# Kernel tuning notes

Hardware: AMD Instinct MI355X
Metric: run time of the kernel (lower is better)

The kernel has to match this reference:

```python
import jax, jax.numpy as jnp
import numpy as np

NUM_E = 20000   # entities
NUM_R = 200     # relations (rel table has 2*NUM_R rows)
H = 200         # h_dim
TD = 48         # t_dim (UnionTimeEncode: two halves of 24)
HD = TD // 2
L_HIST = 32     # padded per-(batch,k) history list length
HIS_K = 3
N_HIST = 3      # len(his_list_g)
N_LAYERS = 2    # RGCN layers (config.num_layers)
E = 200000      # edges per historical graph
BATCH = 512


def setup_inputs() -> dict:
    key = jax.random.key(0)
    ks = jax.random.split(key, 32)
    nrm = lambda k, shape, s=0.05: (jax.random.normal(k, shape, jnp.float32) * s)
    inp = {}
    # graph / index inputs (int)
    inp['src'] = jax.random.randint(ks[0], (N_HIST, E), 0, NUM_E, jnp.int32)
    inp['dst'] = jax.random.randint(ks[1], (N_HIST, E), 0, NUM_E, jnp.int32)
    inp['etype'] = jax.random.randint(ks[2], (N_HIST, E), 0, 2 * NUM_R, jnp.int32)
    inp['data'] = jax.random.randint(ks[3], (BATCH, 4), 0, NUM_R, jnp.int32)  # s,r,o,t
    inp['his_idx'] = jax.random.randint(ks[4], (BATCH, HIS_K, L_HIST), 0, NUM_E, jnp.int32)
    inp['his_len'] = jax.random.randint(ks[5], (BATCH, HIS_K), 0, L_HIST + 1, jnp.int32)
    # parameters (float)
    inp['ent'] = nrm(ks[6], (NUM_E, H), 0.5)          # EntEmb.ent (normal init)
    inp['loop_weight'] = nrm(ks[7], (H, H))           # EntEmb self-loop weight
    inp['rel'] = nrm(ks[8], (2 * NUM_R, H), 0.5)
    # UnionTimeEncode params (AbsTimeEncode v=0 + CosTimeEncode)
    basis = (1.0 / 10 ** np.linspace(0.0, 9.0, HD)).astype(np.float32)
    inp['abs_freq'] = jnp.asarray(basis)
    inp['abs_phase'] = jnp.zeros((HD,), jnp.float32)
    inp['cos_freq'] = jnp.asarray(basis)
    inp['cos_phase'] = jnp.zeros((HD,), jnp.float32)
    # RGCN (RE-GCN style Union-RGCN layer: msg=(h_src+rel_e)@Wn, mean agg, self-loop)
    inp['Wn'] = nrm(ks[9], (N_LAYERS, H, H))
    inp['Ws'] = nrm(ks[10], (N_LAYERS, H, H))
    # GRUCell (PyTorch layout)
    inp['W_ih'] = nrm(ks[11], (3 * H, H + TD))
    inp['W_hh'] = nrm(ks[12], (3 * H, H))
    inp['b_ih'] = jnp.zeros((3 * H,), jnp.float32)
    inp['b_hh'] = jnp.zeros((3 * H,), jnp.float32)
    # attention fusion
    inp['Wb_w'] = nrm(ks[13], (H, 3 * H + TD))
    inp['Wb_b'] = jnp.zeros((H,), jnp.float32)
    inp['Wc_w'] = nrm(ks[14], (1, H))
    inp['Wc_b'] = jnp.zeros((1,), jnp.float32)
    # decoder (MLP query @ entity table)
    inp['Wd_w'] = nrm(ks[15], (H, 3 * H))
    inp['Wd_b'] = jnp.zeros((H,), jnp.float32)
    return inp


def _l2n(x, eps=1e-12):
    # F.normalize: x / max(||x||, eps)
    n = jnp.linalg.norm(x, axis=-1, keepdims=True)
    return x / jnp.maximum(n, eps)


def reference(src, dst, etype, data, his_idx, his_len,
              ent, loop_weight, rel, abs_freq, abs_phase, cos_freq, cos_phase,
              Wn, Ws, W_ih, W_hh, b_ih, b_hh, Wb_w, Wb_b, Wc_w, Wc_b, Wd_w, Wd_b):
    def tenc(t):  # t: [N,1] float -> [N,TD]
        a = jnp.tanh((t + 1.0) * abs_freq + abs_phase)   # AbsTimeEncode(act=tanh)
        c = jnp.cos(t * cos_freq + cos_phase)            # CosTimeEncode
        return jnp.concatenate([a, c], axis=1)

    s_i, r_i = data[:, 0], data[:, 1]
    ent_e = ent @ loop_weight                  # EntEmb self-loop (dropout=identity, eval)
    rel_n = _l2n(rel)
    prev = _l2n(ent_e)                         # g_list[0]
    tim_cnt = N_HIST
    ones_e = jnp.ones((E,), jnp.float32)
    for i in range(N_HIST):                    # python loop over fixed #graphs
        si, di, ei = src[i], dst[i], etype[i]
        deg = jax.ops.segment_sum(ones_e, di, num_segments=NUM_E)         # in-degree
        inv = 1.0 / jnp.maximum(deg, 1.0)
        # g.update_all(copy_src, mean): zero in-degree nodes -> 0
        agg = jax.ops.segment_sum(prev[si], di, num_segments=NUM_E) * inv[:, None]
        h = _l2n(jnp.where(deg[:, None] > 0, agg, 0.0))
        tim_cnt -= 1
        tim = jnp.where(deg > 0, float(tim_cnt), 100.0)[:, None]
        te = tenc(tim)                                                     # [NUM_E,TD]
        for l in range(N_LAYERS):              # RGCN
            msg = (h[si] + rel_n[ei]) @ Wn[l]                              # [E,H]
            nagg = jax.ops.segment_sum(msg, di, num_segments=NUM_E) * inv[:, None]
            h = jax.nn.relu(nagg + h @ Ws[l])
        h = _l2n(h)
        # GRUCell(cat([h, te]), prev)
        gi = jnp.concatenate([h, te], axis=1) @ W_ih.T + b_ih
        gh = prev @ W_hh.T + b_hh
        ir, iz, iN = jnp.split(gi, 3, axis=1)
        hr, hz, hN = jnp.split(gh, 3, axis=1)
        rg = jax.nn.sigmoid(ir + hr)
        zg = jax.nn.sigmoid(iz + hz)
        ng = jnp.tanh(iN + rg * hN)
        prev = _l2n((1.0 - zg) * ng + zg * prev)
    out = prev

    q_s, q_r = out[s_i], rel_n[r_i]
    tim_cnt = min(N_HIST, HIS_K)
    s_embs, atts = [], []
    pos = jnp.arange(L_HIST)[None, :]
    for k in range(min(N_HIST, HIS_K)):
        tim_cnt -= 1
        ln = his_len[:, k]
        mask = (pos < ln[:, None]).astype(jnp.float32)                     # [B,L]
        # sparse one-hot mm + divide by length
        tmp = jnp.einsum('blh,bl->bh', out[his_idx[:, k, :]], mask)
        tmp = _l2n(tmp / jnp.maximum(ln, 1).astype(jnp.float32)[:, None])
        tim = jnp.where(ln > 0, float(tim_cnt), 100.0)[:, None]
        te = tenc(tim)                                                     # [B,TD]
        s_embs.append(tmp)
        a = jax.nn.relu(jnp.concatenate([q_s, q_r, tmp, te], 1) @ Wb_w.T + Wb_b)
        atts.append(a @ Wc_w.T + Wc_b)                                     # [B,1]
    att = jax.nn.softmax(jnp.stack(atts, axis=1), axis=1)                  # [B,K,1]
    out2 = jnp.sum(jnp.stack(s_embs, axis=1) * att, axis=1)                # bmm fusion
    # decoder: MLP query scored against all entity states
    q = jax.nn.relu(jnp.concatenate([q_s, q_r, out2], 1) @ Wd_w.T + Wd_b)
    return q @ out.T                                                       # [B,NUM_E]
```

## Files before the change

kernel.cpp:

```cpp
#include <hip/hip_runtime.h>
#include <hip/hip_bf16.h>

#define NUM_E   20000
#define H_DIM   200
#define TD_DIM  48
#define HD_DIM  24
#define L_HIST  32
#define N_HIST  3
#define E_EDGES 200000
#define BATCH   512


__device__ inline float wave_sum64(float x) {
    #pragma unroll
    for (int m = 1; m < 64; m <<= 1) x += __shfl_xor(x, m);
    return x;
}

__device__ inline ushort f2bf(float f) {
    unsigned u = __float_as_uint(f);
    u += 0x7fffu + ((u >> 16) & 1u);
    return (ushort)(u >> 16);
}
__device__ inline float bf2f(ushort u) {
    return __uint_as_float(((unsigned)u) << 16);
}
__device__ inline float4 bf4_to_f4(ushort4 v) {
    return (float4){bf2f(v.x), bf2f(v.y), bf2f(v.z), bf2f(v.w)};
}

__global__ void fill_i32(int* __restrict__ p, long n, int v) {
    long i = (long)blockIdx.x * blockDim.x + threadIdx.x;
    if (i < n) p[i] = v;
}

__global__ void bias_sum(float* __restrict__ bsum, const float* __restrict__ b_ih,
                         const float* __restrict__ b_hh) {
    int j = blockIdx.x * 256 + threadIdx.x;
    if (j < 600) bsum[j] = b_ih[j] + b_hh[j];
}

__global__ void cvt_bf16_k(ushort* __restrict__ o, const float* __restrict__ in, long n) {
    long i = (long)blockIdx.x * 256 + threadIdx.x;
    if (i < n) o[i] = f2bf(in[i]);
}

__global__ void make_lo(ushort* __restrict__ lo, const float* __restrict__ x,
                        const ushort* __restrict__ hi, long n) {
    long i = (long)blockIdx.x * 256 + threadIdx.x;
    if (i < n) lo[i] = f2bf(x[i] - bf2f(hi[i]));
}

__global__ void tcvt_bf16_k(ushort* __restrict__ o, const float* __restrict__ in, int R, int C) {
    int i = blockIdx.x * 256 + threadIdx.x;
    if (i >= R * C) return;
    int r = i / C, c = i - r * C;
    o[(size_t)c * R + r] = f2bf(in[i]);
}

struct Segs {
    const float* A[4];
    const float* B[4];
    int lda[4], ldb[4], Ks[4];
    int nseg, Ktot;
};

__device__ inline void seg_find(const Segs& sg, int gk, int& s, int& loc) {
    s = 0; loc = gk;
    #pragma unroll
    for (int t = 0; t < 3; t++) {
        if (s + 1 < sg.nseg && loc >= sg.Ks[s]) { loc -= sg.Ks[s]; s++; }
    }
}

__global__ __launch_bounds__(256) void sgemm_splitk(
    float* __restrict__ P, const Segs sg, int M, int N, int nbx, int nby,
    int KS, int tpc)
{
    __shared__ float As[32][68];
    __shared__ float Bs[32][68];

    int tot = nbx * nby;
    int tot_all = tot * KS;
    int chunk = (tot_all + 7) >> 3;
    int v = (int)(blockIdx.x & 7) * chunk + (int)(blockIdx.x >> 3);
    if (v >= tot_all) return;
    int kc = v / tot;
    int tile = v - kc * tot;
    int by = tile / nbx, bx = tile - by * nbx;
    const int bn = bx * 64;
    const int bm = by * 64;
    const int tid = threadIdx.x;
    const int m0 = (tid >> 4) * 4;
    const int n0 = (tid & 15) * 4;

    float acc[4][4];
    #pragma unroll
    for (int i = 0; i < 4; i++)
        #pragma unroll
        for (int j = 0; j < 4; j++) acc[i][j] = 0.f;

    const int Ktot = sg.Ktot;
    const int ntile = (Ktot + 31) / 32;
    const int kt0 = kc * tpc;
    const int kt1 = min(ntile, kt0 + tpc);

    const int a_m  = tid & 31;
    const int a_k4 = (tid >> 5) * 4;
    const int b1_n = tid & 63;
    const int b1_k = (tid >> 6) * 4;

    float4 ra[2], rb[2];
    auto loadA = [&](int k0) {
        int gk = k0 + a_k4;
        bool kin = gk < Ktot;
        int s = 0, loc = 0;
        if (kin) seg_find(sg, gk, s, loc);
        const float* Ab = sg.A[s];
        const int lda = sg.lda[s];
        #pragma unroll
        for (int r = 0; r < 2; r++) {
            int row = bm + a_m + 32 * r;
            float4 vv = {0.f, 0.f, 0.f, 0.f};
            if (kin && row < M) vv = *(const float4*)(Ab + (size_t)row * lda + loc);
            ra[r] = vv;
        }
    };
    auto loadB = [&](int k0) {
        #pragma unroll
        for (int r = 0; r < 2; r++) {
            int k4 = b1_k + 16 * r;
            int gk = k0 + k4;
            bool kin = gk < Ktot;
            int s = 0, loc = 0;
            if (kin) seg_find(sg, gk, s, loc);
            const float* Bb = sg.B[s];
            const int ldb = sg.ldb[s];
            int gn = bn + b1_n;
            float4 vv = {0.f, 0.f, 0.f, 0.f};
            if (kin && gn < N) vv = *(const float4*)(Bb + (size_t)gn * ldb + loc);
            rb[r] = vv;
        }
    };

    if (kt0 < kt1) {
        loadA(kt0 * 32); loadB(kt0 * 32);
        for (int t = kt0; t < kt1; t++) {
            #pragma unroll
            for (int r = 0; r < 2; r++) {
                int m = a_m + 32 * r;
                As[a_k4 + 0][m] = ra[r].x;
                As[a_k4 + 1][m] = ra[r].y;
                As[a_k4 + 2][m] = ra[r].z;
                As[a_k4 + 3][m] = ra[r].w;
            }
            #pragma unroll
            for (int r = 0; r < 2; r++) {
                int k4 = b1_k + 16 * r;
                Bs[k4 + 0][b1_n] = rb[r].x;
                Bs[k4 + 1][b1_n] = rb[r].y;
                Bs[k4 + 2][b1_n] = rb[r].z;
                Bs[k4 + 3][b1_n] = rb[r].w;
            }
            __syncthreads();
            if (t + 1 < kt1) { loadA((t + 1) * 32); loadB((t + 1) * 32); }
            #pragma unroll 8
            for (int kk = 0; kk < 32; kk++) {
                float4 b = *(float4*)&Bs[kk][n0];
                float4 av = *(float4*)&As[kk][m0];
                float a[4] = {av.x, av.y, av.z, av.w};
                #pragma unroll
                for (int i = 0; i < 4; i++) {
                    acc[i][0] += a[i] * b.x;
                    acc[i][1] += a[i] * b.y;
                    acc[i][2] += a[i] * b.z;
                    acc[i][3] += a[i] * b.w;
                }
            }
            __syncthreads();
        }
    }

    int col = bn + n0;
    if (col < N) {
        #pragma unroll
        for (int i = 0; i < 4; i++) {
            int row = bm + m0 + i;
            if (row < M) {
                float4 o = {acc[i][0], acc[i][1], acc[i][2], acc[i][3]};
                *(float4*)(P + ((size_t)kc * M + row) * N + col) = o;
            }
        }
    }
}

__global__ void reduce_relu(float* __restrict__ out, const float* __restrict__ P,
                            const float* __restrict__ bias, int MN, int N, int KS)
{
    int i = blockIdx.x * 256 + threadIdx.x;
    if (i >= MN) return;
    float s = bias[i % N];
    for (int k = 0; k < KS; k++) s += P[(size_t)k * MN + i];
    out[i] = fmaxf(s, 0.f);
}

__global__ void reduce_relu_split(ushort* __restrict__ qhi, ushort* __restrict__ qlo,
                                  const float* __restrict__ P, const float* __restrict__ bias,
                                  int MN, int N, int KS)
{
    int i = blockIdx.x * 256 + threadIdx.x;
    if (i >= MN) return;
    float s = bias[i % N];
    for (int k = 0; k < KS; k++) s += P[(size_t)k * MN + i];
    s = fmaxf(s, 0.f);
    ushort h = f2bf(s);
    qhi[i] = h;
    qlo[i] = f2bf(s - bf2f(h));
}

typedef __attribute__((ext_vector_type(8))) short bfrag;
typedef __attribute__((ext_vector_type(4))) float ffrag;

struct BfSegs {
    const ushort* A[3];
    const ushort* B[3];
    int lda[3], ldb[3], Ks[3];
    int nseg, Ktot;
};

__device__ inline void bseg_find(const BfSegs& sg, int gk, int& s, int& loc) {
    s = 0; loc = gk;
    #pragma unroll
    for (int t = 0; t < 2; t++) {
        if (s + 1 < sg.nseg && loc >= sg.Ks[s]) { loc -= sg.Ks[s]; s++; }
    }
}

struct GemmDesc {
    BfSegs sg;
    float* C;
    ushort* Cb;
    const float* bias;
    int M, N, ldc;
    int act, flags, order;
    int nbx, nby, blk0, nblk;
};

struct MultiArgs {
    GemmDesc d[3];
    int nd;
    int tot;
};

template<int DI>
__device__ __forceinline__ void gemm_body(const MultiArgs& ma, int v,
                                          ushort* __restrict__ Als,
                                          ushort* __restrict__ Bls)
{
    const GemmDesc& D = ma.d[DI];
    const BfSegs& sg = D.sg;
    const int tile = v - D.blk0;
    int by, bx;
    if (D.order == 0) { by = tile / D.nbx; bx = tile - by * D.nbx; }
    else              { bx = tile / D.nby; by = tile - bx * D.nby; }
    const int bm = by * 64, bn = bx * 64;
    const int M = D.M, N = D.N;

    const int tid  = threadIdx.x;
    const int lane = tid & 63;
    const int w    = tid >> 6;
    const int wm   = (w & 1) * 2;
    const int wn   = (w >> 1) * 2;

    ffrag acc[2][2];
    #pragma unroll
    for (int i = 0; i < 2; i++)
        #pragma unroll
        for (int j = 0; j < 2; j++) acc[i][j] = (ffrag){0.f, 0.f, 0.f, 0.f};

    const int Ktot = sg.Ktot;
    const int nkt = (Ktot + 63) >> 6;

    int a_m[2], a_kq[2], a_wc[2];
    #pragma unroll
    for (int i = 0; i < 2; i++) {
        int c = i * 256 + tid;
        a_m[i] = c & 63; a_kq[i] = c >> 6;
        a_wc[i] = ((a_m[i] >> 4) * 2 + (a_kq[i] >> 2)) * 64 + (a_kq[i] & 3) * 16 + (a_m[i] & 15);
    }
    int b_n[2], b_kq[2], b_wc[2];
    #pragma unroll
    for (int i = 0; i < 2; i++) {
        int c = i * 256 + tid;
        b_n[i] = c & 63; b_kq[i] = c >> 6;
        b_wc[i] = ((b_n[i] >> 4) * 2 + (b_kq[i] >> 2)) * 64 + (b_kq[i] & 3) * 16 + (b_n[i] & 15);
    }

    uint4 ra[2], rb[2];
    auto loadA = [&](int k0) {
        #pragma unroll
        for (int i = 0; i < 2; i++) {
            int gk = k0 + a_kq[i] * 8;
            int row = bm + a_m[i];
            uint4 vv = {0u, 0u, 0u, 0u};
            if (gk < Ktot && row < M) {
                int s, loc; bseg_find(sg, gk, s, loc);
                vv = *(const uint4*)(sg.A[s] + (size_t)row * sg.lda[s] + loc);
            }
            ra[i] = vv;
        }
    };
    auto loadB = [&](int k0) {
        #pragma unroll
        for (int i = 0; i < 2; i++) {
            int gk = k0 + b_kq[i] * 8;
            int gn = bn + b_n[i];
            uint4 vv = {0u, 0u, 0u, 0u};
            if (gk < Ktot && gn < N) {
                int s, loc; bseg_find(sg, gk, s, loc);
                vv = *(const uint4*)(sg.B[s] + (size_t)gn * sg.ldb[s] + loc);
            }
            rb[i] = vv;
        }
    };

    loadA(0); loadB(0);

    for (int t = 0; t < nkt; t++) {
        #pragma unroll
        for (int i = 0; i < 2; i++) *(uint4*)(&Als[a_wc[i] * 8]) = ra[i];
        #pragma unroll
        for (int i = 0; i < 2; i++) *(uint4*)(&Bls[b_wc[i] * 8]) = rb[i];
        __syncthreads();

        if (t + 1 < nkt) { loadA((t + 1) << 6); loadB((t + 1) << 6); }

        #pragma unroll
        for (int kt = 0; kt < 2; kt++) {
            bfrag af[2], bf[2];
            #pragma unroll
            for (int i = 0; i < 2; i++)
                af[i] = *(const bfrag*)(&Als[(((wm + i) * 2 + kt) * 64 + lane) * 8]);
            #pragma unroll
            for (int j = 0; j < 2; j++)
                bf[j] = *(const bfrag*)(&Bls[(((wn + j) * 2 + kt) * 64 + lane) * 8]);
            #pragma unroll
            for (int i = 0; i < 2; i++)
                #pragma unroll
                for (int j = 0; j < 2; j++)
                    acc[i][j] = __builtin_amdgcn_mfma_f32_16x16x32_bf16(af[i], bf[j], acc[i][j], 0, 0, 0);
        }
        __syncthreads();
    }

    const int rbase = (lane >> 4) * 4;
    const int cl = lane & 15;
    #pragma unroll
    for (int j = 0; j < 2; j++) {
        int col = bn + (wn + j) * 16 + cl;
        if (col >= N) continue;
        float bv = D.bias ? D.bias[col] : 0.f;
        #pragma unroll
        for (int i = 0; i < 2; i++) {
            int mrow = bm + (wm + i) * 16 + rbase;
            #pragma unroll
            for (int r = 0; r < 4; r++) {
                int row = mrow + r;
                if (row < M) {
                    float o = acc[i][j][r] + bv;
                    if (D.act == 1) o = fmaxf(o, 0.f);
                    else if (D.act == 2) o = 1.f / (1.f + expf(-o));
                    if (D.flags & 1) D.C[(size_t)row * D.ldc + col] = o;
                    if (D.flags & 2) D.Cb[(size_t)row * D.ldc + col] = f2bf(o);
                }
            }
        }
    }
}

__global__ __launch_bounds__(256) void mfma_multi(MultiArgs ma)
{
    __shared__ __align__(16) ushort Als[4096];
    __shared__ __align__(16) ushort Bls[4096];

    int tot = ma.tot;
    int chunk = (tot + 7) >> 3;
    int v = (int)(blockIdx.x & 7) * chunk + (int)(blockIdx.x >> 3);
    if (v >= tot) return;

    int di = 0;
    if (ma.nd > 1 && v >= ma.d[1].blk0) di = 1;
    if (ma.nd > 2 && v >= ma.d[2].blk0) di = 2;

    if (di == 0)      gemm_body<0>(ma, v, Als, Bls);
    else if (di == 1) gemm_body<1>(ma, v, Als, Bls);
    else              gemm_body<2>(ma, v, Als, Bls);
}


__global__ void count_dst(const int* __restrict__ di, int* __restrict__ cnt, int E) {
    int e = blockIdx.x * 256 + threadIdx.x;
    if (e < E) atomicAdd(&cnt[di[e]], 1);
}

__global__ __launch_bounds__(1024) void scan_rows(
    const int* __restrict__ cnt, int* __restrict__ row_start, int* __restrict__ cursor,
    float* __restrict__ degf, float* __restrict__ invd)
{
    __shared__ int part[1024];
    const int CH = (NUM_E + 1023) / 1024;
    int t = threadIdx.x;
    int base = t * CH;
    int local[32];
    int s = 0;
    for (int j = 0; j < CH; j++) {
        int idx = base + j;
        int c = (idx < NUM_E) ? cnt[idx] : 0;
        local[j] = s; s += c;
    }
    part[t] = s;
    __syncthreads();
    for (int off = 1; off < 1024; off <<= 1) {
        int vv = (t >= off) ? part[t - off] : 0;
        __syncthreads();
        part[t] += vv;
        __syncthreads();
    }
    int pre = (t == 0) ? 0 : part[t - 1];
    for (int j = 0; j < CH; j++) {
        int idx = base + j;
        if (idx < NUM_E) {
            int rs = pre + local[j];
            row_start[idx] = rs;
            cursor[idx] = rs;
            int c = cnt[idx];
            degf[idx] = (float)c;
            invd[idx] = 1.f / fmaxf((float)c, 1.f);
        }
    }
    if (t == 1023) row_start[NUM_E] = part[1023];
}

__global__ void build_perm(const int* __restrict__ si, const int* __restrict__ di,
                           const int* __restrict__ ei, int* __restrict__ cursor,
                           int* __restrict__ ssrc, int* __restrict__ setype, int E)
{
    int e = blockIdx.x * 256 + threadIdx.x;
    if (e >= E) return;
    int pos = atomicAdd(&cursor[di[e]], 1);
    ssrc[pos]   = si[e];
    setype[pos] = ei[e];
}


__global__ __launch_bounds__(256) void seg_gather_norm_bf(
    ushort* __restrict__ bh, const ushort* __restrict__ bprev,
    const int* __restrict__ ssrc, const int* __restrict__ row_start,
    const float* __restrict__ invd)
{
    int v = blockIdx.x * 4 + (threadIdx.x >> 6);
    int lane = threadIdx.x & 63;
    if (v >= NUM_E) return;
    int s0 = row_start[v], s1 = row_start[v + 1];
    bool act = lane < 50;
    float4 acc = {0.f, 0.f, 0.f, 0.f};
    int j = s0;
    for (; j + 1 < s1; j += 2) {
        int sa = ssrc[j], sb = ssrc[j + 1];
        if (act) {
            float4 xa = bf4_to_f4(*(const ushort4*)(bprev + (long)sa * H_DIM + lane * 4));
            float4 xb = bf4_to_f4(*(const ushort4*)(bprev + (long)sb * H_DIM + lane * 4));
            acc.x += xa.x + xb.x; acc.y += xa.y + xb.y;
            acc.z += xa.z + xb.z; acc.w += xa.w + xb.w;
        }
    }
    if (j < s1) {
        int sa = ssrc[j];
        if (act) {
            float4 xa = bf4_to_f4(*(const ushort4*)(bprev + (long)sa * H_DIM + lane * 4));
            acc.x += xa.x; acc.y += xa.y; acc.z += xa.z; acc.w += xa.w;
        }
    }
    float iv = invd[v];
    acc.x *= iv; acc.y *= iv; acc.z *= iv; acc.w *= iv;
    float ss = act ? (acc.x*acc.x + acc.y*acc.y + acc.z*acc.z + acc.w*acc.w) : 0.f;
    ss = wave_sum64(ss);
    float r = 1.f / fmaxf(sqrtf(ss), 1e-12f);
    if (act) {
        ushort4 ob = {f2bf(acc.x * r), f2bf(acc.y * r), f2bf(acc.z * r), f2bf(acc.w * r)};
        *(ushort4*)(bh + (long)v * H_DIM + lane * 4) = ob;
    }
}

__global__ __launch_bounds__(256) void seg_gather_layer_bf(
    ushort* __restrict__ btmp, const ushort* __restrict__ bh, const ushort* __restrict__ brel,
    const int* __restrict__ ssrc, const int* __restrict__ setype,
    const int* __restrict__ row_start, const float* __restrict__ invd)
{
    int v = blockIdx.x * 4 + (threadIdx.x >> 6);
    int lane = threadIdx.x & 63;
    if (v >= NUM_E) return;
    int s0 = row_start[v], s1 = row_start[v + 1];
    bool act = lane < 50;
    float4 acc = {0.f, 0.f, 0.f, 0.f};
    int j = s0;
    for (; j + 1 < s1; j += 2) {
        int sa = ssrc[j], ta = setype[j];
        int sb = ssrc[j + 1], tb = setype[j + 1];
        if (act) {
            float4 xa = bf4_to_f4(*(const ushort4*)(bh   + (long)sa * H_DIM + lane * 4));
            float4 ya = bf4_to_f4(*(const ushort4*)(brel + (long)ta * H_DIM + lane * 4));
            float4 xb = bf4_to_f4(*(const ushort4*)(bh   + (long)sb * H_DIM + lane * 4));
            float4 yb = bf4_to_f4(*(const ushort4*)(brel + (long)tb * H_DIM + lane * 4));
            acc.x += (xa.x + ya.x) + (xb.x + yb.x);
            acc.y += (xa.y + ya.y) + (xb.y + yb.y);
            acc.z += (xa.z + ya.z) + (xb.z + yb.z);
            acc.w += (xa.w + ya.w) + (xb.w + yb.w);
        }
    }
    if (j < s1) {
        int s = ssrc[j];
        int t = setype[j];
        if (act) {
            float4 x = bf4_to_f4(*(const ushort4*)(bh   + (long)s * H_DIM + lane * 4));
            float4 y = bf4_to_f4(*(const ushort4*)(brel + (long)t * H_DIM + lane * 4));
            acc.x += x.x + y.x; acc.y += x.y + y.y;
            acc.z += x.z + y.z; acc.w += x.w + y.w;
        }
    }
    float iv = invd[v];
    if (act) {
        ushort4 ob = {f2bf(acc.x * iv), f2bf(acc.y * iv), f2bf(acc.z * iv), f2bf(acc.w * iv)};
        *(ushort4*)(btmp + (long)v * H_DIM + lane * 4) = ob;
    }
}


__global__ __launch_bounds__(256) void l2norm_rows4(
    float* __restrict__ out, ushort* __restrict__ bout,
    const float* __restrict__ in, int nrows)
{
    int v = blockIdx.x * 4 + (threadIdx.x >> 6);
    int lane = threadIdx.x & 63;
    if (v >= nrows) return;
    bool act = lane < 50;
    float4 x = {0.f, 0.f, 0.f, 0.f};
    if (act) x = *(const float4*)(in + (long)v * H_DIM + lane * 4);
    float ss = x.x*x.x + x.y*x.y + x.z*x.z + x.w*x.w;
    ss = wave_sum64(ss);
    float r = 1.f / fmaxf(sqrtf(ss), 1e-12f);
    if (act) {
        long base = (long)v * H_DIM + lane * 4;
        float4 o = {x.x * r, x.y * r, x.z * r, x.w * r};
        *(float4*)(out + base) = o;
        if (bout) {
            ushort4 ob = {f2bf(o.x), f2bf(o.y), f2bf(o.z), f2bf(o.w)};
            *(ushort4*)(bout + base) = ob;
        }
    }
}

__global__ __launch_bounds__(256) void l2norm_bf4(ushort* __restrict__ b, int nrows)
{
    int v = blockIdx.x * 4 + (threadIdx.x >> 6);
    int lane = threadIdx.x & 63;
    if (v >= nrows) return;
    bool act = lane < 50;
    float4 x = {0.f, 0.f, 0.f, 0.f};
    long base = (long)v * H_DIM + lane * 4;
    if (act) x = bf4_to_f4(*(const ushort4*)(b + base));
    float ss = x.x*x.x + x.y*x.y + x.z*x.z + x.w*x.w;
    ss = wave_sum64(ss);
    float r = 1.f / fmaxf(sqrtf(ss), 1e-12f);
    if (act) {
        ushort4 ob = {f2bf(x.x * r), f2bf(x.y * r), f2bf(x.z * r), f2bf(x.w * r)};
        *(ushort4*)(b + base) = ob;
    }
}

__global__ void tenc_table(ushort* __restrict__ tbl, const float* __restrict__ af,
                           const float* __restrict__ ap, const float* __restrict__ cf,
                           const float* __restrict__ cp, float tcnt)
{
    int j = threadIdx.x;
    if (j >= 128) return;
    int half = j >> 6;
    int jj = j & 63;
    if (jj >= TD_DIM) return;
    float t = half ? 100.0f : tcnt;
    float val;
    if (jj < HD_DIM) val = tanhf((t + 1.f) * af[jj] + ap[jj]);
    else             val = cosf(t * cf[jj - HD_DIM] + cp[jj - HD_DIM]);
    tbl[half * 64 + jj] = f2bf(val);
}

__global__ void tenc_fill(ushort* __restrict__ bte, const float* __restrict__ deg,
                          const ushort* __restrict__ tbl, int M)
{
    int idx = blockIdx.x * 256 + threadIdx.x;
    if (idx >= M * 6) return;
    int v = idx / 6, c = idx - v * 6;
    int base = (deg[v] > 0.f) ? 0 : 64;
    *(uint4*)(bte + (long)v * TD_DIM + c * 8) = *(const uint4*)(tbl + base + c * 8);
}

__global__ __launch_bounds__(256) void gru_fused(
    float* __restrict__ prev, ushort* __restrict__ bprev, const float* __restrict__ rz,
    const float* __restrict__ iN, const float* __restrict__ hN)
{
    int v = blockIdx.x * 4 + (threadIdx.x >> 6);
    int lane = threadIdx.x & 63;
    if (v >= NUM_E) return;
    bool act = lane < 50;
    long b200 = (long)v * H_DIM + lane * 4;
    long b400 = (long)v * 400 + lane * 4;
    float4 o = {0.f, 0.f, 0.f, 0.f};
    if (act) {
        float4 r4 = *(const float4*)(rz + b400);
        float4 z4 = *(const float4*)(rz + b400 + 200);
        float4 n4 = *(const float4*)(iN + b200);
        float4 g4 = *(const float4*)(hN + b200);
        float4 p4 = *(const float4*)(prev + b200);
        float ngx = tanhf(n4.x + r4.x * g4.x);
        float ngy = tanhf(n4.y + r4.y * g4.y);
        float ngz = tanhf(n4.z + r4.z * g4.z);
        float ngw = tanhf(n4.w + r4.w * g4.w);
        o.x = (1.f - z4.x) * ngx + z4.x * p4.x;
        o.y = (1.f - z4.y) * ngy + z4.y * p4.y;
        o.z = (1.f - z4.z) * ngz + z4.z * p4.z;
        o.w = (1.f - z4.w) * ngw + z4.w * p4.w;
    }
    float ss = o.x*o.x + o.y*o.y + o.z*o.z + o.w*o.w;
    ss = wave_sum64(ss);
    float r = 1.f / fmaxf(sqrtf(ss), 1e-12f);
    if (act) {
        float4 wv = {o.x * r, o.y * r, o.z * r, o.w * r};
        *(float4*)(prev + b200) = wv;
        ushort4 ob = {f2bf(wv.x), f2bf(wv.y), f2bf(wv.z), f2bf(wv.w)};
        *(ushort4*)(bprev + b200) = ob;
    }
}


__global__ void gather_qs_qr3(float* __restrict__ qs3, float* __restrict__ qr3,
                              const float* __restrict__ out, const float* __restrict__ reln,
                              const int* __restrict__ data)
{
    long i = (long)blockIdx.x * 256 + threadIdx.x;
    if (i >= (long)BATCH * H_DIM) return;
    int b = (int)(i / H_DIM), j = (int)(i % H_DIM);
    float vs = out[(long)data[b * 4 + 0] * H_DIM + j];
    float vr = reln[(long)data[b * 4 + 1] * H_DIM + j];
    const long S = (long)BATCH * H_DIM;
    qs3[i] = vs; qs3[i + S] = vs; qs3[i + 2*S] = vs;
    qr3[i] = vr; qr3[i + S] = vr; qr3[i + 2*S] = vr;
}

__global__ __launch_bounds__(64) void semb_kernel(
    float* __restrict__ semb, const float* __restrict__ out,
    const int* __restrict__ his_idx, const int* __restrict__ his_len)
{
    int b = blockIdx.x, k = blockIdx.y;
    int lane = threadIdx.x;
    int ln = his_len[b * 3 + k];
    if (ln > L_HIST) ln = L_HIST;
    float vals[4] = {0.f, 0.f, 0.f, 0.f};
    for (int l = 0; l < ln; l++) {
        int idx = his_idx[((long)b * 3 + k) * L_HIST + l];
        #pragma unroll
        for (int t = 0; t < 4; t++) {
            int j = lane + t * 64;
            if (j < H_DIM) vals[t] += out[(long)idx * H_DIM + j];
        }
    }
    float scale = 1.f / fmaxf((float)ln, 1.f);
    float ss = 0.f;
    #pragma unroll
    for (int t = 0; t < 4; t++) { vals[t] *= scale; ss += vals[t] * vals[t]; }
    ss = wave_sum64(ss);
    float r = 1.f / fmaxf(sqrtf(ss), 1e-12f);
    #pragma unroll
    for (int t = 0; t < 4; t++) {
        int j = lane + t * 64;
        if (j < H_DIM) semb[((long)k * BATCH + b) * H_DIM + j] = vals[t] * r;
    }
}

__global__ void tenc_batch(float* __restrict__ teb, const int* __restrict__ his_len,
                           const float* __restrict__ af, const float* __restrict__ ap,
                           const float* __restrict__ cf, const float* __restrict__ cp)
{
    int idx = blockIdx.x * 256 + threadIdx.x;
    if (idx >= 3 * BATCH * TD_DIM) return;
    int k = idx / (BATCH * TD_DIM);
    int rem = idx - k * (BATCH * TD_DIM);
    int b = rem / TD_DIM, j = rem % TD_DIM;
    int ln = his_len[b * 3 + k];
    float t = (ln > 0) ? (float)(2 - k) : 100.0f;
    float val;
    if (j < HD_DIM) val = tanhf((t + 1.f) * af[j] + ap[j]);
    else            val = cosf(t * cf[j - HD_DIM] + cp[j - HD_DIM]);
    teb[idx] = val;
}

__global__ __launch_bounds__(256) void att_logits_rows(
    float* __restrict__ atts, const float* __restrict__ a,
    const float* __restrict__ Wc_w, const float* __restrict__ Wc_b)
{
    int row = blockIdx.x * 4 + (threadIdx.x >> 6);
    int lane = threadIdx.x & 63;
    if (row >= 3 * BATCH) return;
    int k = row >> 9;
    int b = row & 511;
    float s = 0.f;
    for (int j = lane; j < H_DIM; j += 64) s += a[(long)row * H_DIM + j] * Wc_w[j];
    s = wave_sum64(s);
    if (lane == 0) atts[b * 3 + k] = s + Wc_b[0];
}

__global__ void softmax_out2(float* __restrict__ out2, const float* __restrict__ atts,
                             const float* __restrict__ semb)
{
    long i = (long)blockIdx.x * 256 + threadIdx.x;
    if (i >= (long)BATCH * H_DIM) return;
    int b = (int)(i / H_DIM), j = (int)(i % H_DIM);
    float l0 = atts[b * 3 + 0], l1 = atts[b * 3 + 1], l2 = atts[b * 3 + 2];
    float m = fmaxf(l0, fmaxf(l1, l2));
    float e0 = expf(l0 - m), e1 = expf(l1 - m), e2 = expf(l2 - m);
    float s = e0 + e1 + e2;
    float v = (e0 * semb[((long)0 * BATCH + b) * H_DIM + j] +
               e1 * semb[((long)1 * BATCH + b) * H_DIM + j] +
               e2 * semb[((long)2 * BATCH + b) * H_DIM + j]) / s;
    out2[i] = v;
}


extern "C" void kernel_launch(void* const* d_in, const int* in_sizes, int n_in,
                              void* d_out, int out_size, void* d_ws, size_t ws_size,
                              hipStream_t stream)
{
    (void)in_sizes; (void)n_in; (void)out_size; (void)ws_size;

    const int*   src     = (const int*)d_in[0];
    const int*   dst     = (const int*)d_in[1];
    const int*   etype   = (const int*)d_in[2];
    const int*   data    = (const int*)d_in[3];
    const int*   his_idx = (const int*)d_in[4];
    const int*   his_len = (const int*)d_in[5];
    const float* ent     = (const float*)d_in[6];
    const float* loop_w  = (const float*)d_in[7];
    const float* rel     = (const float*)d_in[8];
    const float* af      = (const float*)d_in[9];
    const float* ap      = (const float*)d_in[10];
    const float* cf      = (const float*)d_in[11];
    const float* cp      = (const float*)d_in[12];
    const float* Wn      = (const float*)d_in[13];
    const float* Ws      = (const float*)d_in[14];
    const float* W_ih    = (const float*)d_in[15];
    const float* W_hh    = (const float*)d_in[16];
    const float* b_ih    = (const float*)d_in[17];
    const float* b_hh    = (const float*)d_in[18];
    const float* Wb_w    = (const float*)d_in[19];
    const float* Wb_b    = (const float*)d_in[20];
    const float* Wc_w    = (const float*)d_in[21];
    const float* Wc_b    = (const float*)d_in[22];
    const float* Wd_w    = (const float*)d_in[23];
    const float* Wd_b    = (const float*)d_in[24];
    float* out_p = (float*)d_out;

    float* wp = (float*)d_ws;
    size_t off = 0;
    auto alloc = [&](size_t n) {
        size_t n4 = (n + 3) & ~(size_t)3;
        float* p = wp + off; off += n4; return p;
    };
    const long nE200 = (long)NUM_E * H_DIM;
    float* prev   = alloc(nE200);
    float* h1     = alloc(nE200);
    float* tmp    = alloc(nE200);
    float* rz     = out_p;
    ushort* bh0   = (ushort*)alloc(nE200 / 2);
    ushort* bh1   = (ushort*)alloc(nE200 / 2);
    ushort* btmp  = (ushort*)alloc(nE200 / 2);
    ushort* bprev = (ushort*)alloc(nE200 / 2);
    ushort* plo   = (ushort*)alloc(nE200 / 2);
    ushort* bte   = (ushort*)alloc((size_t)NUM_E * TD_DIM / 2);
    ushort* brel  = (ushort*)alloc(400 * H_DIM / 2);
    ushort* bW_ih = (ushort*)alloc(600 * 248 / 2);
    ushort* bW_hh = (ushort*)alloc(600 * 200 / 2);
    ushort* bWn_t = (ushort*)alloc(2 * 200 * 200 / 2);
    ushort* bWs_t = (ushort*)alloc(2 * 200 * 200 / 2);
    ushort* bLp_t = (ushort*)alloc(200 * 200 / 2);
    ushort* qhi   = (ushort*)alloc(BATCH * H_DIM / 2);
    ushort* qlo   = (ushort*)alloc(BATCH * H_DIM / 2);
    ushort* ttbl  = (ushort*)alloc(64);
    float* degf   = alloc(NUM_E);
    float* invd   = alloc(NUM_E);
    float* reln   = alloc(400 * H_DIM);
    float* bsum   = alloc(1024);
    float* qs3    = alloc(3 * BATCH * H_DIM);
    float* qr3    = alloc(3 * BATCH * H_DIM);
    float* semb   = alloc(3 * BATCH * H_DIM);
    float* teb    = alloc(3 * BATCH * TD_DIM);
    float* abuf   = alloc(3 * BATCH * H_DIM);
    float* atts   = alloc(2048);
    float* out2   = alloc(BATCH * H_DIM);
    int* cnt       = (int*)alloc(NUM_E);
    int* row_start = (int*)alloc(NUM_E + 4);
    int* cursor    = (int*)alloc(NUM_E);
    int* ssrc      = (int*)alloc(E_EDGES);
    int* setype    = (int*)alloc(E_EDGES);

    auto nblk = [](long n) { return (unsigned)((n + 255) / 256); };

    auto bseg1 = [](const ushort* A, int la, const ushort* B, int lb, int K) {
        BfSegs s{}; s.A[0]=A; s.lda[0]=la; s.B[0]=B; s.ldb[0]=lb; s.Ks[0]=K;
        s.nseg=1; s.Ktot=K; return s;
    };
    auto bseg2 = [](const ushort* A0, int la0, const ushort* B0, int lb0, int K0,
                    const ushort* A1, int la1, const ushort* B1, int lb1, int K1) {
        BfSegs s{}; s.A[0]=A0; s.lda[0]=la0; s.B[0]=B0; s.ldb[0]=lb0; s.Ks[0]=K0;
        s.A[1]=A1; s.lda[1]=la1; s.B[1]=B1; s.ldb[1]=lb1; s.Ks[1]=K1;
        s.nseg=2; s.Ktot=K0+K1; return s;
    };
    auto bseg3 = [](const ushort* A0, int la0, const ushort* B0, int lb0, int K0,
                    const ushort* A1, int la1, const ushort* B1, int lb1, int K1,
                    const ushort* A2, int la2, const ushort* B2, int lb2, int K2) {
        BfSegs s{}; s.A[0]=A0; s.lda[0]=la0; s.B[0]=B0; s.ldb[0]=lb0; s.Ks[0]=K0;
        s.A[1]=A1; s.lda[1]=la1; s.B[1]=B1; s.ldb[1]=lb1; s.Ks[1]=K1;
        s.A[2]=A2; s.lda[2]=la2; s.B[2]=B2; s.ldb[2]=lb2; s.Ks[2]=K2;
        s.nseg=3; s.Ktot=K0+K1+K2; return s;
    };

    auto desc = [](const BfSegs& sg, float* C, ushort* Cb, const float* bias,
                   int M, int N, int ldc, int act, int flags, int order) {
        GemmDesc D{}; D.sg=sg; D.C=C; D.Cb=Cb; D.bias=bias;
        D.M=M; D.N=N; D.ldc=ldc; D.act=act; D.flags=flags; D.order=order;
        D.nbx=(N+63)>>6; D.nby=(M+63)>>6; D.nblk=D.nbx*D.nby; D.blk0=0;
        return D;
    };
    auto launch_multi = [&](GemmDesc* ds, int nd) {
        MultiArgs ma{};
        int tot = 0;
        for (int i = 0; i < nd; i++) { ds[i].blk0 = tot; tot += ds[i].nblk; ma.d[i] = ds[i]; }
        ma.nd = nd; ma.tot = tot;
        unsigned grid = (unsigned)(((tot + 7) >> 3) << 3);
        mfma_multi<<<grid, 256, 0, stream>>>(ma);
    };

    auto seg3 = [](const float* A0, int la0, const float* B0, int lb0, int K0,
                   const float* A1, int la1, const float* B1, int lb1, int K1,
                   const float* A2, int la2, const float* B2, int lb2, int K2) {
        Segs s{}; s.A[0]=A0; s.lda[0]=la0; s.B[0]=B0; s.ldb[0]=lb0; s.Ks[0]=K0;
        s.A[1]=A1; s.lda[1]=la1; s.B[1]=B1; s.ldb[1]=lb1; s.Ks[1]=K1;
        s.A[2]=A2; s.lda[2]=la2; s.B[2]=B2; s.ldb[2]=lb2; s.Ks[2]=K2;
        s.nseg=3; s.Ktot=K0+K1+K2; return s;
    };
    auto seg4 = [](const float* A0, int la0, const float* B0, int lb0, int K0,
                   const float* A1, int la1, const float* B1, int lb1, int K1,
                   const float* A2, int la2, const float* B2, int lb2, int K2,
                   const float* A3, int la3, const float* B3, int lb3, int K3) {
        Segs s{}; s.A[0]=A0; s.lda[0]=la0; s.B[0]=B0; s.ldb[0]=lb0; s.Ks[0]=K0;
        s.A[1]=A1; s.lda[1]=la1; s.B[1]=B1; s.ldb[1]=lb1; s.Ks[1]=K1;
        s.A[2]=A2; s.lda[2]=la2; s.B[2]=B2; s.ldb[2]=lb2; s.Ks[2]=K2;
        s.A[3]=A3; s.lda[3]=la3; s.B[3]=B3; s.ldb[3]=lb3; s.Ks[3]=K3;
        s.nseg=4; s.Ktot=K0+K1+K2+K3; return s;
    };
    auto splitk = [&](float* P, const Segs& sg, int M, int N, int KS) {
        int nbx = (N + 63) >> 6;
        int nby = (M + 63) >> 6;
        int ntile = (sg.Ktot + 31) / 32;
        int tpc = (ntile + KS - 1) / KS;
        int tot_all = nbx * nby * KS;
        unsigned grid = (unsigned)(((tot_all + 7) >> 3) << 3);
        sgemm_splitk<<<grid, 256, 0, stream>>>(P, sg, M, N, nbx, nby, KS, tpc);
    };

    const unsigned r4 = (NUM_E + 3) / 4;

    l2norm_rows4<<<100, 256, 0, stream>>>(reln, brel, rel, 400);
    bias_sum<<<3, 256, 0, stream>>>(bsum, b_ih, b_hh);
    cvt_bf16_k<<<nblk(600L*248), 256, 0, stream>>>(bW_ih, W_ih, 600L*248);
    cvt_bf16_k<<<nblk(600L*200), 256, 0, stream>>>(bW_hh, W_hh, 600L*200);
    tcvt_bf16_k<<<nblk(40000), 256, 0, stream>>>(bLp_t, loop_w, 200, 200);
    tcvt_bf16_k<<<nblk(40000), 256, 0, stream>>>(bWn_t,          Wn,          200, 200);
    tcvt_bf16_k<<<nblk(40000), 256, 0, stream>>>(bWn_t + 40000,  Wn + 40000,  200, 200);
    tcvt_bf16_k<<<nblk(40000), 256, 0, stream>>>(bWs_t,          Ws,          200, 200);
    tcvt_bf16_k<<<nblk(40000), 256, 0, stream>>>(bWs_t + 40000,  Ws + 40000,  200, 200);

    cvt_bf16_k<<<nblk(nE200), 256, 0, stream>>>(btmp, ent, nE200);
    {
        GemmDesc d0 = desc(bseg1(btmp, H_DIM, bLp_t, H_DIM, H_DIM),
                           tmp, nullptr, nullptr, NUM_E, H_DIM, H_DIM, 0, 1, 0);
        launch_multi(&d0, 1);
    }
    l2norm_rows4<<<r4, 256, 0, stream>>>(prev, bprev, tmp, NUM_E);

    for (int i = 0; i < N_HIST; i++) {
        const int* si = src   + (long)i * E_EDGES;
        const int* di = dst   + (long)i * E_EDGES;
        const int* ei = etype + (long)i * E_EDGES;
        float tcnt = (float)(N_HIST - 1 - i);

        fill_i32<<<nblk(NUM_E), 256, 0, stream>>>(cnt, NUM_E, 0);
        count_dst<<<nblk(E_EDGES), 256, 0, stream>>>(di, cnt, E_EDGES);
        scan_rows<<<1, 1024, 0, stream>>>(cnt, row_start, cursor, degf, invd);
        build_perm<<<nblk(E_EDGES), 256, 0, stream>>>(si, di, ei, cursor, ssrc, setype, E_EDGES);

        seg_gather_norm_bf<<<r4, 256, 0, stream>>>(bh0, bprev, ssrc, row_start, invd);
        tenc_table<<<1, 128, 0, stream>>>(ttbl, af, ap, cf, cp, tcnt);
        tenc_fill<<<nblk((long)NUM_E * 6), 256, 0, stream>>>(bte, degf, ttbl, NUM_E);

        seg_gather_layer_bf<<<r4, 256, 0, stream>>>(btmp, bh0, brel, ssrc, setype, row_start, invd);
        {
            GemmDesc d0 = desc(bseg2(btmp, H_DIM, bWn_t,         H_DIM, H_DIM,
                                     bh0,  H_DIM, bWs_t,         H_DIM, H_DIM),
                               nullptr, bh1, nullptr, NUM_E, H_DIM, H_DIM, 1, 2, 0);
            launch_multi(&d0, 1);
        }
        seg_gather_layer_bf<<<r4, 256, 0, stream>>>(btmp, bh1, brel, ssrc, setype, row_start, invd);
        {
            GemmDesc d0 = desc(bseg2(btmp, H_DIM, bWn_t + 40000, H_DIM, H_DIM,
                                     bh1,  H_DIM, bWs_t + 40000, H_DIM, H_DIM),
                               nullptr, bh0, nullptr, NUM_E, H_DIM, H_DIM, 1, 2, 0);
            launch_multi(&d0, 1);
        }
        l2norm_bf4<<<r4, 256, 0, stream>>>(bh0, NUM_E);

        {
            GemmDesc d3[3];
            d3[0] = desc(bseg3(bh0,   H_DIM,  bW_ih,       248, H_DIM,
                               bte,   TD_DIM, bW_ih + 200, 248, TD_DIM,
                               bprev, H_DIM,  bW_hh,       200, H_DIM),
                         rz, nullptr, bsum, NUM_E, 400, 400, 2, 1, 0);
            d3[1] = desc(bseg2(bh0, H_DIM,  bW_ih + 400*248,       248, H_DIM,
                               bte, TD_DIM, bW_ih + 400*248 + 200, 248, TD_DIM),
                         h1, nullptr, b_ih + 400, NUM_E, H_DIM, H_DIM, 0, 1, 0);
            d3[2] = desc(bseg1(bprev, H_DIM, bW_hh + 400*200, 200, H_DIM),
                         tmp, nullptr, b_hh + 400, NUM_E, H_DIM, H_DIM, 0, 1, 0);
            launch_multi(d3, 3);
        }

        gru_fused<<<r4, 256, 0, stream>>>(prev, bprev, rz, h1, tmp);
    }

    gather_qs_qr3<<<nblk((long)BATCH * H_DIM), 256, 0, stream>>>(qs3, qr3, prev, reln, data);
    semb_kernel<<<dim3(BATCH, 3), 64, 0, stream>>>(semb, prev, his_idx, his_len);
    tenc_batch<<<nblk(3L * BATCH * TD_DIM), 256, 0, stream>>>(teb, his_len, af, ap, cf, cp);

    {
        const int KS = 8;
        const int MN = 3 * BATCH * H_DIM;
        splitk(h1, seg4(qs3, H_DIM,  Wb_w,       648, H_DIM,
                        qr3, H_DIM,  Wb_w + 200, 648, H_DIM,
                        semb, H_DIM, Wb_w + 400, 648, H_DIM,
                        teb, TD_DIM, Wb_w + 600, 648, TD_DIM),
               3 * BATCH, H_DIM, KS);
        reduce_relu<<<nblk(MN), 256, 0, stream>>>(abuf, h1, Wb_b, MN, H_DIM, KS);
    }
    att_logits_rows<<<(3 * BATCH + 3) / 4, 256, 0, stream>>>(atts, abuf, Wc_w, Wc_b);
    softmax_out2<<<nblk((long)BATCH * H_DIM), 256, 0, stream>>>(out2, atts, semb);

    {
        const int KS = 8;
        const int MN = BATCH * H_DIM;
        splitk(tmp, seg3(qs3, H_DIM,  Wd_w,       600, H_DIM,
                         qr3, H_DIM,  Wd_w + 200, 600, H_DIM,
                         out2, H_DIM, Wd_w + 400, 600, H_DIM),
               BATCH, H_DIM, KS);
        reduce_relu_split<<<nblk(MN), 256, 0, stream>>>(qhi, qlo, tmp, Wd_b, MN, H_DIM, KS);
    }

    make_lo<<<nblk(nE200), 256, 0, stream>>>(plo, prev, bprev, nE200);

    {
        GemmDesc d0 = desc(bseg3(qhi, H_DIM, bprev, H_DIM, H_DIM,
                                 qhi, H_DIM, plo,   H_DIM, H_DIM,
                                 qlo, H_DIM, bprev, H_DIM, H_DIM),
                           out_p, nullptr, nullptr, BATCH, NUM_E, NUM_E, 0, 1, 1);
        launch_multi(&d0, 1);
    }
}
```

Baseline: 1.230 ms.

## Double-buffer GEMM global loads in registers and use lighter barriers

The bf16 MFMA GEMM kernel now keeps two sets of register staging buffers, so global loads for tile t+2 are in flight while tile t is computed. The loop is unrolled by two. The full __syncthreads is replaced by an explicit lgkmcnt wait plus s_barrier, which does not wait on outstanding global loads. The aim is to hide global memory latency across the K loop, at the cost of extra registers, which may reduce occupancy. The asm barriers also depend on correct wait semantics for LDS.

```diff
diff --git a/kernel.cpp b/kernel.cpp
--- a/kernel.cpp
+++ b/kernel.cpp
@@ -296,8 +296,8 @@
         b_wc[i] = ((b_n[i] >> 4) * 2 + (b_kq[i] >> 2)) * 64 + (b_kq[i] & 3) * 16 + (b_n[i] & 15);
     }
 
-    uint4 ra[2], rb[2];
-    auto loadA = [&](int k0) {
+    uint4 ra0[2], rb0[2], ra1[2], rb1[2];
+    auto loadA = [&](int k0, uint4* r) {
         #pragma unroll
         for (int i = 0; i < 2; i++) {
             int gk = k0 + a_kq[i] * 8;
@@ -307,10 +307,10 @@
                 int s, loc; bseg_find(sg, gk, s, loc);
                 vv = *(const uint4*)(sg.A[s] + (size_t)row * sg.lda[s] + loc);
             }
-            ra[i] = vv;
-        }
-    };
-    auto loadB = [&](int k0) {
+            r[i] = vv;
+        }
+    };
+    auto loadB = [&](int k0, uint4* r) {
         #pragma unroll
         for (int i = 0; i < 2; i++) {
             int gk = k0 + b_kq[i] * 8;
@@ -320,21 +320,11 @@
                 int s, loc; bseg_find(sg, gk, s, loc);
                 vv = *(const uint4*)(sg.B[s] + (size_t)gn * sg.ldb[s] + loc);
             }
-            rb[i] = vv;
-        }
-    };
-
-    loadA(0); loadB(0);
-
-    for (int t = 0; t < nkt; t++) {
-        #pragma unroll
-        for (int i = 0; i < 2; i++) *(uint4*)(&Als[a_wc[i] * 8]) = ra[i];
-        #pragma unroll
-        for (int i = 0; i < 2; i++) *(uint4*)(&Bls[b_wc[i] * 8]) = rb[i];
-        __syncthreads();
-
-        if (t + 1 < nkt) { loadA((t + 1) << 6); loadB((t + 1) << 6); }
-
+            r[i] = vv;
+        }
+    };
+
+    auto compute = [&]() {
         #pragma unroll
         for (int kt = 0; kt < 2; kt++) {
             bfrag af[2], bf[2];
@@ -350,7 +340,35 @@
                 for (int j = 0; j < 2; j++)
                     acc[i][j] = __builtin_amdgcn_mfma_f32_16x16x32_bf16(af[i], bf[j], acc[i][j], 0, 0, 0);
         }
-        __syncthreads();
+    };
+
+    loadA(0, ra0);  loadB(0, rb0);
+    loadA(64, ra1); loadB(64, rb1);
+
+    for (int t = 0; t < nkt; t += 2) {
+        #pragma unroll
+        for (int i = 0; i < 2; i++) *(uint4*)(&Als[a_wc[i] * 8]) = ra0[i];
+        #pragma unroll
+        for (int i = 0; i < 2; i++) *(uint4*)(&Bls[b_wc[i] * 8]) = rb0[i];
+        asm volatile("s_waitcnt lgkmcnt(0)" ::: "memory");
+        __builtin_amdgcn_s_barrier();
+        if (t + 2 < nkt) { loadA((t + 2) << 6, ra0); loadB((t + 2) << 6, rb0); }
+        compute();
+        asm volatile("s_waitcnt lgkmcnt(0)" ::: "memory");
+        __builtin_amdgcn_s_barrier();
+
+        if (t + 1 >= nkt) break;
+
+        #pragma unroll
+        for (int i = 0; i < 2; i++) *(uint4*)(&Als[a_wc[i] * 8]) = ra1[i];
+        #pragma unroll
+        for (int i = 0; i < 2; i++) *(uint4*)(&Bls[b_wc[i] * 8]) = rb1[i];
+        asm volatile("s_waitcnt lgkmcnt(0)" ::: "memory");
+        __builtin_amdgcn_s_barrier();
+        if (t + 3 < nkt) { loadA((t + 3) << 6, ra1); loadB((t + 3) << 6, rb1); }
+        compute();
+        asm volatile("s_waitcnt lgkmcnt(0)" ::: "memory");
+        __builtin_amdgcn_s_barrier();
     }
 
     const int rbase = (lane >> 4) * 4;
```

New measurement: 1.350 ms. 9.8% more time.

## Batch CSR construction and time-encoding for all three graphs up front

Applied to the files above, without the earlier changes.

The per-graph CSR build steps (count, scan, permutation) and the time-encoding table and fill kernels are hoisted out of the history loop. Each now runs once over all three graphs, with buffers sized for three graphs. This cuts the number of kernel launches and gives the small kernels three times more parallel work, including three scan blocks instead of one. The cost is extra workspace memory for the per-graph CSR arrays and time encodings.

```diff
diff --git a/kernel.cpp b/kernel.cpp
--- a/kernel.cpp
+++ b/kernel.cpp
@@ -398,16 +398,27 @@
 }
 
 
-__global__ void count_dst(const int* __restrict__ di, int* __restrict__ cnt, int E) {
-    int e = blockIdx.x * 256 + threadIdx.x;
-    if (e < E) atomicAdd(&cnt[di[e]], 1);
-}
-
-__global__ __launch_bounds__(1024) void scan_rows(
-    const int* __restrict__ cnt, int* __restrict__ row_start, int* __restrict__ cursor,
-    float* __restrict__ degf, float* __restrict__ invd)
+__global__ void count_dst3(const int* __restrict__ dst, int* __restrict__ cnt) {
+    long e = (long)blockIdx.x * 256 + threadIdx.x;
+    if (e < (long)N_HIST * E_EDGES) {
+        int g = (int)(e / E_EDGES);
+        atomicAdd(&cnt[g * NUM_E + dst[e]], 1);
+    }
+}
+
+__global__ __launch_bounds__(1024) void scan_rows3(
+    const int* __restrict__ cnt_all, int* __restrict__ row_start_all,
+    int* __restrict__ cursor_all, float* __restrict__ degf_all,
+    float* __restrict__ invd_all)
 {
     __shared__ int part[1024];
+    const int g = blockIdx.x;
+    const int* cnt = cnt_all + g * NUM_E;
+    int* row_start  = row_start_all + g * (NUM_E + 4);
+    int* cursor     = cursor_all + g * NUM_E;
+    float* degf     = degf_all + g * NUM_E;
+    float* invd     = invd_all + g * NUM_E;
+
     const int CH = (NUM_E + 1023) / 1024;
     int t = threadIdx.x;
     int base = t * CH;
@@ -441,15 +452,16 @@
     if (t == 1023) row_start[NUM_E] = part[1023];
 }
 
-__global__ void build_perm(const int* __restrict__ si, const int* __restrict__ di,
-                           const int* __restrict__ ei, int* __restrict__ cursor,
-                           int* __restrict__ ssrc, int* __restrict__ setype, int E)
-{
-    int e = blockIdx.x * 256 + threadIdx.x;
-    if (e >= E) return;
-    int pos = atomicAdd(&cursor[di[e]], 1);
-    ssrc[pos]   = si[e];
-    setype[pos] = ei[e];
+__global__ void build_perm3(const int* __restrict__ src, const int* __restrict__ dst,
+                            const int* __restrict__ etype, int* __restrict__ cursor_all,
+                            int* __restrict__ ssrc_all, int* __restrict__ setype_all)
+{
+    long e = (long)blockIdx.x * 256 + threadIdx.x;
+    if (e >= (long)N_HIST * E_EDGES) return;
+    int g = (int)(e / E_EDGES);
+    int pos = atomicAdd(&cursor_all[g * NUM_E + dst[e]], 1);
+    ssrc_all[(long)g * E_EDGES + pos]   = src[e];
+    setype_all[(long)g * E_EDGES + pos] = etype[e];
 }
 
 
@@ -578,30 +590,36 @@
     }
 }
 
-__global__ void tenc_table(ushort* __restrict__ tbl, const float* __restrict__ af,
-                           const float* __restrict__ ap, const float* __restrict__ cf,
-                           const float* __restrict__ cp, float tcnt)
-{
-    int j = threadIdx.x;
-    if (j >= 128) return;
-    int half = j >> 6;
-    int jj = j & 63;
+__global__ void tenc_table3(ushort* __restrict__ tbl, const float* __restrict__ af,
+                            const float* __restrict__ ap, const float* __restrict__ cf,
+                            const float* __restrict__ cp)
+{
+    int j = blockIdx.x * 256 + threadIdx.x;
+    if (j >= 384) return;
+    int g = j >> 7;
+    int r = j & 127;
+    int half = r >> 6;
+    int jj = r & 63;
     if (jj >= TD_DIM) return;
+    float tcnt = (float)(N_HIST - 1 - g);
     float t = half ? 100.0f : tcnt;
     float val;
     if (jj < HD_DIM) val = tanhf((t + 1.f) * af[jj] + ap[jj]);
     else             val = cosf(t * cf[jj - HD_DIM] + cp[jj - HD_DIM]);
-    tbl[half * 64 + jj] = f2bf(val);
-}
-
-__global__ void tenc_fill(ushort* __restrict__ bte, const float* __restrict__ deg,
-                          const ushort* __restrict__ tbl, int M)
-{
-    int idx = blockIdx.x * 256 + threadIdx.x;
-    if (idx >= M * 6) return;
-    int v = idx / 6, c = idx - v * 6;
-    int base = (deg[v] > 0.f) ? 0 : 64;
-    *(uint4*)(bte + (long)v * TD_DIM + c * 8) = *(const uint4*)(tbl + base + c * 8);
+    tbl[g * 128 + half * 64 + jj] = f2bf(val);
+}
+
+__global__ void tenc_fill3(ushort* __restrict__ bte3, const float* __restrict__ degf_all,
+                           const ushort* __restrict__ tbl)
+{
+    long idx = (long)blockIdx.x * 256 + threadIdx.x;
+    if (idx >= (long)N_HIST * NUM_E * 6) return;
+    int g = (int)(idx / (NUM_E * 6));
+    int rem = (int)(idx - (long)g * NUM_E * 6);
+    int v = rem / 6, c = rem - v * 6;
+    int base = (degf_all[g * NUM_E + v] > 0.f) ? 0 : 64;
+    *(uint4*)(bte3 + ((long)g * NUM_E + v) * TD_DIM + c * 8) =
+        *(const uint4*)(tbl + g * 128 + base + c * 8);
 }
 
 __global__ __launch_bounds__(256) void gru_fused(
@@ -784,7 +802,7 @@
     ushort* btmp  = (ushort*)alloc(nE200 / 2);
     ushort* bprev = (ushort*)alloc(nE200 / 2);
     ushort* plo   = (ushort*)alloc(nE200 / 2);
-    ushort* bte   = (ushort*)alloc((size_t)NUM_E * TD_DIM / 2);
+    ushort* bte3  = (ushort*)alloc((size_t)N_HIST * NUM_E * TD_DIM / 2);
     ushort* brel  = (ushort*)alloc(400 * H_DIM / 2);
     ushort* bW_ih = (ushort*)alloc(600 * 248 / 2);
     ushort* bW_hh = (ushort*)alloc(600 * 200 / 2);
@@ -793,9 +811,9 @@
     ushort* bLp_t = (ushort*)alloc(200 * 200 / 2);
     ushort* qhi   = (ushort*)alloc(BATCH * H_DIM / 2);
     ushort* qlo   = (ushort*)alloc(BATCH * H_DIM / 2);
-    ushort* ttbl  = (ushort*)alloc(64);
-    float* degf   = alloc(NUM_E);
-    float* invd   = alloc(NUM_E);
+    ushort* ttbl  = (ushort*)alloc(256);
+    float* degf   = alloc(3 * NUM_E);
+    float* invd   = alloc(3 * NUM_E);
     float* reln   = alloc(400 * H_DIM);
     float* bsum   = alloc(1024);
     float* qs3    = alloc(3 * BATCH * H_DIM);
@@ -805,11 +823,11 @@
     float* abuf   = alloc(3 * BATCH * H_DIM);
     float* atts   = alloc(2048);
     float* out2   = alloc(BATCH * H_DIM);
-    int* cnt       = (int*)alloc(NUM_E);
-    int* row_start = (int*)alloc(NUM_E + 4);
-    int* cursor    = (int*)alloc(NUM_E);
-    int* ssrc      = (int*)alloc(E_EDGES);
-    int* setype    = (int*)alloc(E_EDGES);
+    int* cnt       = (int*)alloc(3 * NUM_E);
+    int* row_start = (int*)alloc(3 * (NUM_E + 4));
+    int* cursor    = (int*)alloc(3 * NUM_E);
+    int* ssrc      = (int*)alloc(3L * E_EDGES);
+    int* setype    = (int*)alloc(3L * E_EDGES);
 
     auto nblk = [](long n) { return (unsigned)((n + 255) / 256); };
 
@@ -888,6 +906,13 @@
     tcvt_bf16_k<<<nblk(40000), 256, 0, stream>>>(bWs_t,          Ws,          200, 200);
     tcvt_bf16_k<<<nblk(40000), 256, 0, stream>>>(bWs_t + 40000,  Ws + 40000,  200, 200);
 
+    fill_i32<<<nblk(3L * NUM_E), 256, 0, stream>>>(cnt, 3L * NUM_E, 0);
+    count_dst3<<<nblk(3L * E_EDGES), 256, 0, stream>>>(dst, cnt);
+    scan_rows3<<<3, 1024, 0, stream>>>(cnt, row_start, cursor, degf, invd);
+    build_perm3<<<nblk(3L * E_EDGES), 256, 0, stream>>>(src, dst, etype, cursor, ssrc, setype);
+    tenc_table3<<<2, 256, 0, stream>>>(ttbl, af, ap, cf, cp);
+    tenc_fill3<<<nblk(3L * NUM_E * 6), 256, 0, stream>>>(bte3, degf, ttbl);
+
     cvt_bf16_k<<<nblk(nE200), 256, 0, stream>>>(btmp, ent, nE200);
     {
         GemmDesc d0 = desc(bseg1(btmp, H_DIM, bLp_t, H_DIM, H_DIM),
@@ -897,28 +922,22 @@
     l2norm_rows4<<<r4, 256, 0, stream>>>(prev, bprev, tmp, NUM_E);
 
     for (int i = 0; i < N_HIST; i++) {
-        const int* si = src   + (long)i * E_EDGES;
-        const int* di = dst   + (long)i * E_EDGES;
-        const int* ei = etype + (long)i * E_EDGES;
-        float tcnt = (float)(N_HIST - 1 - i);
-
-        fill_i32<<<nblk(NUM_E), 256, 0, stream>>>(cnt, NUM_E, 0);
-        count_dst<<<nblk(E_EDGES), 256, 0, stream>>>(di, cnt, E_EDGES);
-        scan_rows<<<1, 1024, 0, stream>>>(cnt, row_start, cursor, degf, invd);
-        build_perm<<<nblk(E_EDGES), 256, 0, stream>>>(si, di, ei, cursor, ssrc, setype, E_EDGES);
-
-        seg_gather_norm_bf<<<r4, 256, 0, stream>>>(bh0, bprev, ssrc, row_start, invd);
-        tenc_table<<<1, 128, 0, stream>>>(ttbl, af, ap, cf, cp, tcnt);
-        tenc_fill<<<nblk((long)NUM_E * 6), 256, 0, stream>>>(bte, degf, ttbl, NUM_E);
-
-        seg_gather_layer_bf<<<r4, 256, 0, stream>>>(btmp, bh0, brel, ssrc, setype, row_start, invd);
+        const int* ssrc_g = ssrc + (long)i * E_EDGES;
+        const int* sety_g = setype + (long)i * E_EDGES;
+        const int* rs_g   = row_start + i * (NUM_E + 4);
+        const float* iv_g = invd + i * NUM_E;
+        ushort* bte_g     = bte3 + (long)i * NUM_E * TD_DIM;
+
+        seg_gather_norm_bf<<<r4, 256, 0, stream>>>(bh0, bprev, ssrc_g, rs_g, iv_g);
+
+        seg_gather_layer_bf<<<r4, 256, 0, stream>>>(btmp, bh0, brel, ssrc_g, sety_g, rs_g, iv_g);
         {
             GemmDesc d0 = desc(bseg2(btmp, H_DIM, bWn_t,         H_DIM, H_DIM,
                                      bh0,  H_DIM, bWs_t,         H_DIM, H_DIM),
                                nullptr, bh1, nullptr, NUM_E, H_DIM, H_DIM, 1, 2, 0);
             launch_multi(&d0, 1);
         }
-        seg_gather_layer_bf<<<r4, 256, 0, stream>>>(btmp, bh1, brel, ssrc, setype, row_start, invd);
+        seg_gather_layer_bf<<<r4, 256, 0, stream>>>(btmp, bh1, brel, ssrc_g, sety_g, rs_g, iv_g);
         {
             GemmDesc d0 = desc(bseg2(btmp, H_DIM, bWn_t + 40000, H_DIM, H_DIM,
                                      bh1,  H_DIM, bWs_t + 40000, H_DIM, H_DIM),
@@ -930,11 +949,11 @@
         {
             GemmDesc d3[3];
             d3[0] = desc(bseg3(bh0,   H_DIM,  bW_ih,       248, H_DIM,
-                               bte,   TD_DIM, bW_ih + 200, 248, TD_DIM,
+                               bte_g, TD_DIM, bW_ih + 200, 248, TD_DIM,
                                bprev, H_DIM,  bW_hh,       200, H_DIM),
                          rz, nullptr, bsum, NUM_E, 400, 400, 2, 1, 0);
-            d3[1] = desc(bseg2(bh0, H_DIM,  bW_ih + 400*248,       248, H_DIM,
-                               bte, TD_DIM, bW_ih + 400*248 + 200, 248, TD_DIM),
+            d3[1] = desc(bseg2(bh0,   H_DIM,  bW_ih + 400*248,       248, H_DIM,
+                               bte_g, TD_DIM, bW_ih + 400*248 + 200, 248, TD_DIM),
                          h1, nullptr, b_ih + 400, NUM_E, H_DIM, H_DIM, 0, 1, 0);
             d3[2] = desc(bseg1(bprev, H_DIM, bW_hh + 400*200, 200, H_DIM),
                          tmp, nullptr, b_hh + 400, NUM_E, H_DIM, H_DIM, 0, 1, 0);
```

Measured after the change: 1.096 ms (median of 2 runs). 1.12x faster.
